# Kernel tuning notes

Hardware: AMD Instinct MI355X
Metric: run time of the kernel (lower is better)

Reference implementation:

```python
import jax, jax.numpy as jnp
import numpy as np

SPATIAL = ((100, 134), (50, 67), (25, 34), (13, 17))
LEN = sum(h * w for h, w in SPATIAL)   # 17821
D, H, L, P = 384, 8, 4, 4
DH = D // H                            # 48
U = D // 3                             # unit_dim = 128
EPS = 1e-5


def _ln(x, g, b):
    m = jnp.mean(x, -1, keepdims=True)
    v = jnp.mean((x - m) ** 2, -1, keepdims=True)
    return (x - m) * jax.lax.rsqrt(v + EPS) * g + b


def _ffn(t, w1, b1, w2, b2, g, b):
    t2 = jax.nn.relu(t @ w1.T + b1) @ w2.T + b2
    return _ln(t + t2, g, b)


def _msda_core(value, loc, attn):
    # value [B,Lv,H,DH]; loc [B,Lq,H,L,P,2] normalized to [0,1]; attn [B,Lq,H,L,P]
    B = value.shape[0]
    Lq = loc.shape[1]
    out = jnp.zeros((B, H, Lq, DH), value.dtype)
    start = 0
    for lvl, (Hl, Wl) in enumerate(SPATIAL):
        n = Hl * Wl
        v = value[:, start:start + n].transpose(0, 2, 1, 3)        # [B,H,n,DH]
        # grid_sample(align_corners=False) semantics: pixel coord = loc*W - 0.5
        x = loc[:, :, :, lvl, :, 0] * Wl - 0.5                      # [B,Lq,H,P]
        y = loc[:, :, :, lvl, :, 1] * Hl - 0.5
        x0 = jnp.floor(x); y0 = jnp.floor(y)
        dx = x - x0; dy = y - y0
        x0i = x0.astype(jnp.int32); y0i = y0.astype(jnp.int32)
        acc = jnp.zeros((B, H, Lq, P, DH), value.dtype)
        corners = ((0, 0, (1 - dx) * (1 - dy)), (1, 0, dx * (1 - dy)),
                   (0, 1, (1 - dx) * dy), (1, 1, dx * dy))
        for ox, oy, w in corners:
            xi = x0i + ox; yi = y0i + oy
            valid = ((xi >= 0) & (xi < Wl) & (yi >= 0) & (yi < Hl)).astype(value.dtype)
            idx = jnp.clip(yi, 0, Hl - 1) * Wl + jnp.clip(xi, 0, Wl - 1)
            idx_t = idx.transpose(0, 2, 1, 3).reshape(B, H, Lq * P)
            g = jnp.take_along_axis(v, idx_t[..., None], axis=2).reshape(B, H, Lq, P, DH)
            acc = acc + g * (w * valid).transpose(0, 2, 1, 3)[..., None]
        out = out + (acc * attn[:, :, :, lvl].transpose(0, 2, 1, 3)[..., None]).sum(axis=3)
        start += n
    return out.transpose(0, 2, 1, 3).reshape(B, Lq, D)


def setup_inputs() -> dict:
    key = jax.random.key(0)
    ks = jax.random.split(key, 16)
    rn = lambda k, s, sc=1.0: jax.random.normal(k, s, jnp.float32) * sc
    inp = {}
    inp['src'] = rn(ks[0], (1, LEN, D))
    inp['space_query'] = rn(ks[1], (1, 1, 2 * U))
    inp['chann_query'] = rn(ks[2], (1, 1, 2 * U))
    inp['pos'] = rn(ks[3], (1, LEN, D))
    inp['reference_points'] = jax.random.uniform(ks[4], (1, LEN, L, 2), jnp.float32)
    inp['spatial_shapes'] = jnp.array(SPATIAL, jnp.int32)
    starts = np.cumsum([0] + [h * w for h, w in SPATIAL[:-1]])
    inp['level_start_index'] = jnp.array(starts, jnp.int32)
    inp['padding_mask'] = jnp.zeros((1, LEN), bool)
    # MSDeformAttn params (torch Linear convention: W is [out_features, in_features])
    inp['W_off'] = rn(ks[5], (H * L * P * 2, D), 0.01)
    inp['b_off'] = rn(ks[6], (H * L * P * 2,), 0.1)
    inp['W_attn'] = rn(ks[7], (H * L * P, D), D ** -0.5)
    inp['b_attn'] = jnp.zeros((H * L * P,), jnp.float32)
    inp['W_val'] = rn(ks[8], (D, D), D ** -0.5)
    inp['b_val'] = jnp.zeros((D,), jnp.float32)
    inp['W_out'] = rn(ks[9], (D, D), D ** -0.5)
    inp['b_out'] = jnp.zeros((D,), jnp.float32)
    # norm1_xy / norm1_zd
    inp['g1xy'] = jnp.ones((2 * U,), jnp.float32); inp['b1xy'] = jnp.zeros((2 * U,), jnp.float32)
    inp['g1zd'] = jnp.ones((U,), jnp.float32); inp['b1zd'] = jnp.zeros((U,), jnp.float32)
    # ffn_xy: Linear(2U,2U) -> relu -> Linear(2U,2U), residual + LN
    inp['fxy_w1'] = rn(ks[10], (2 * U, 2 * U), (2 * U) ** -0.5); inp['fxy_b1'] = jnp.zeros((2 * U,), jnp.float32)
    inp['fxy_w2'] = rn(ks[11], (2 * U, 2 * U), (2 * U) ** -0.5); inp['fxy_b2'] = jnp.zeros((2 * U,), jnp.float32)
    inp['fxy_g'] = jnp.ones((2 * U,), jnp.float32); inp['fxy_b'] = jnp.zeros((2 * U,), jnp.float32)
    # ffn_zd: Linear(U,U) -> relu -> Linear(U,U), residual + LN
    inp['fzd_w1'] = rn(ks[12], (U, U), U ** -0.5); inp['fzd_b1'] = jnp.zeros((U,), jnp.float32)
    inp['fzd_w2'] = rn(ks[13], (U, U), U ** -0.5); inp['fzd_b2'] = jnp.zeros((U,), jnp.float32)
    inp['fzd_g'] = jnp.ones((U,), jnp.float32); inp['fzd_b'] = jnp.zeros((U,), jnp.float32)
    return inp


def reference(src, space_query, chann_query, pos, reference_points, spatial_shapes,
              level_start_index, padding_mask,
              W_off, b_off, W_attn, b_attn, W_val, b_val, W_out, b_out,
              g1xy, b1xy, g1zd, b1zd,
              fxy_w1, fxy_b1, fxy_w2, fxy_b2, fxy_g, fxy_b,
              fzd_w1, fzd_b1, fzd_w2, fzd_b2, fzd_g, fzd_b):
    B, Lq, _ = src.shape
    q = src + pos                                        # with_pos_embed
    value = src @ W_val.T + b_val
    value = jnp.where(padding_mask[..., None], 0.0, value).reshape(B, Lq, H, DH)
    off = (q @ W_off.T + b_off).reshape(B, Lq, H, L, P, 2)
    attn = jax.nn.softmax((q @ W_attn.T + b_attn).reshape(B, Lq, H, L * P), -1)
    attn = attn.reshape(B, Lq, H, L, P)
    wh = jnp.array([[w, h] for h, w in SPATIAL], src.dtype)         # [L,2] as (W,H)
    loc = reference_points[:, :, None, :, None, :] + off / wh[None, None, None, :, None, :]
    src2 = _msda_core(value, loc, attn) @ W_out.T + b_out
    src_xy = _ln(src[..., :2 * U] + src2[..., :2 * U], g1xy, b1xy)
    src_zd = _ln(src[..., 2 * U:] + src2[..., 2 * U:], g1zd, b1zd)
    src_xy = _ffn(src_xy, fxy_w1, fxy_b1, fxy_w2, fxy_b2, fxy_g, fxy_b)
    src_zd = _ffn(src_zd, fzd_w1, fzd_b1, fzd_w2, fzd_b2, fzd_g, fzd_b)
    return jnp.concatenate([src_xy, src_zd], axis=-1)
```

## Files before the change

### kernel.cpp

```cpp
#include <hip/hip_runtime.h>
#include <math.h>

#define LEN 17821
#define DMODEL 384
#define NHEAD 8
#define DHEAD 48
#define WSZ (384 * 384)

typedef float floatx4 __attribute__((ext_vector_type(4)));
typedef short shortx8 __attribute__((ext_vector_type(8)));
typedef unsigned short ushort;

__device__ inline ushort f2bf(float f) {
    unsigned int u = __float_as_uint(f);
    u += 0x7FFFu + ((u >> 16) & 1u);
    return (ushort)(u >> 16);
}
__device__ inline float bf2f(ushort s) {
    return __uint_as_float(((unsigned int)s) << 16);
}

__global__ __launch_bounds__(256)
void prep_w(const float* __restrict__ Wval, const float* __restrict__ Woff,
            const float* __restrict__ Wattn, const float* __restrict__ Wout,
            const float* __restrict__ w1xy, const float* __restrict__ w1zd,
            const float* __restrict__ w2xy, const float* __restrict__ w2zd,
            ushort* __restrict__ wv, ushort* __restrict__ woa,
            ushort* __restrict__ wo, ushort* __restrict__ w1b,
            ushort* __restrict__ w2b) {
    int idx = blockIdx.x * 256 + threadIdx.x;
    if (idx >= WSZ) return;
    int n = idx / 384, k = idx - n * 384;
    int job = blockIdx.y;
    float v; ushort* dst;
    if (job == 0) { v = Wval[idx]; dst = wv; }
    else if (job == 1) {
        v = n < 256 ? Woff[n * 384 + k] : Wattn[(n - 256) * 384 + k];
        dst = woa;
    } else if (job == 2) { v = Wout[idx]; dst = wo; }
    else if (job == 3) {
        v = n < 256 ? (k < 256 ? w1xy[n * 256 + k] : 0.f)
                    : (k >= 256 ? w1zd[(n - 256) * 128 + (k - 256)] : 0.f);
        dst = w1b;
    } else {
        v = n < 256 ? (k < 256 ? w2xy[n * 256 + k] : 0.f)
                    : (k >= 256 ? w2zd[(n - 256) * 128 + (k - 256)] : 0.f);
        dst = w2b;
    }
    dst[idx] = f2bf(v);
}

__global__ __launch_bounds__(384)
void prep_b(const float* __restrict__ boff, const float* __restrict__ battn,
            const float* __restrict__ b1xy, const float* __restrict__ b1zd,
            const float* __restrict__ b2xy, const float* __restrict__ b2zd,
            const float* __restrict__ g1xy, const float* __restrict__ be1xy,
            const float* __restrict__ g1zd, const float* __restrict__ be1zd,
            const float* __restrict__ g2xy, const float* __restrict__ be2xy,
            const float* __restrict__ g2zd, const float* __restrict__ be2zd,
            float* __restrict__ boa, float* __restrict__ b1c,
            float* __restrict__ b2c, float* __restrict__ l1g,
            float* __restrict__ l1b, float* __restrict__ l2g,
            float* __restrict__ l2b) {
    int i = threadIdx.x;
    bool lo = i < 256; int j = lo ? i : i - 256;
    boa[i] = lo ? boff[i] : battn[j];
    b1c[i] = lo ? b1xy[i] : b1zd[j];
    b2c[i] = lo ? b2xy[i] : b2zd[j];
    l1g[i] = lo ? g1xy[i] : g1zd[j];
    l1b[i] = lo ? be1xy[i] : be1zd[j];
    l2g[i] = lo ? g2xy[i] : g2zd[j];
    l2b[i] = lo ? be2xy[i] : be2zd[j];
}

__global__ __launch_bounds__(256)
void cvt_add(const float* __restrict__ src, const float* __restrict__ pos,
             ushort* __restrict__ src_bf, ushort* __restrict__ q_bf, int n8) {
    int i = blockIdx.x * 256 + threadIdx.x;
    if (i >= n8) return;
    float4 s0 = ((const float4*)src)[i * 2], s1 = ((const float4*)src)[i * 2 + 1];
    float4 p0 = ((const float4*)pos)[i * 2], p1 = ((const float4*)pos)[i * 2 + 1];
    shortx8 sb, qb;
    sb[0] = f2bf(s0.x); sb[1] = f2bf(s0.y); sb[2] = f2bf(s0.z); sb[3] = f2bf(s0.w);
    sb[4] = f2bf(s1.x); sb[5] = f2bf(s1.y); sb[6] = f2bf(s1.z); sb[7] = f2bf(s1.w);
    qb[0] = f2bf(s0.x + p0.x); qb[1] = f2bf(s0.y + p0.y);
    qb[2] = f2bf(s0.z + p0.z); qb[3] = f2bf(s0.w + p0.w);
    qb[4] = f2bf(s1.x + p1.x); qb[5] = f2bf(s1.y + p1.y);
    qb[6] = f2bf(s1.z + p1.z); qb[7] = f2bf(s1.w + p1.w);
    ((shortx8*)src_bf)[i] = sb;
    ((shortx8*)q_bf)[i] = qb;
}

#define TSV 128
#define LSTRIDE 40

__global__ __launch_bounds__(256)
void vq_gemm(const ushort* __restrict__ sbq, const ushort* __restrict__ qbq,
             const ushort* __restrict__ wv, const ushort* __restrict__ woa,
             const float* __restrict__ bval, const float* __restrict__ boa,
             ushort* __restrict__ vout, float* __restrict__ oaout) {
    __shared__ ushort As[TSV * LSTRIDE];
    __shared__ ushort Ws[TSV * LSTRIDE];
    bool job = blockIdx.x >= 3;
    int bx = job ? blockIdx.x - 3 : blockIdx.x;
    const ushort* A = job ? qbq : sbq;
    const ushort* W = job ? woa : wv;
    const float* bias = job ? boa : bval;
    int tid = threadIdx.x;
    int lane = tid & 63, wave = tid >> 6;
    int wr = (wave >> 1) * 64, wc = (wave & 1) * 64;
    int l15 = lane & 15, quad = lane >> 4;
    int srow = tid >> 1, shalf = tid & 1;
    int by = blockIdx.y;
    int garow = by * TSV + srow;
    bool avalid = garow < LEN;
    const ushort* ap = A + (size_t)(avalid ? garow : 0) * 384 + shalf * 16;
    const ushort* wp = W + (size_t)(bx * TSV + srow) * 384 + shalf * 16;
    ushort* as_dst = &As[srow * LSTRIDE + shalf * 16];
    ushort* ws_dst = &Ws[srow * LSTRIDE + shalf * 16];

    floatx4 acc[4][4];
    #pragma unroll
    for (int i = 0; i < 4; ++i)
        #pragma unroll
        for (int j = 0; j < 4; ++j)
            acc[i][j] = (floatx4){0.f, 0.f, 0.f, 0.f};

    shortx8 a0 = *(const shortx8*)(ap);
    shortx8 a1 = *(const shortx8*)(ap + 8);
    shortx8 w0 = *(const shortx8*)(wp);
    shortx8 w1 = *(const shortx8*)(wp + 8);

    for (int k0 = 0; k0 < 384; k0 += 32) {
        __syncthreads();
        *(shortx8*)(as_dst + 0) = a0;
        *(shortx8*)(as_dst + 8) = a1;
        *(shortx8*)(ws_dst + 0) = w0;
        *(shortx8*)(ws_dst + 8) = w1;
        __syncthreads();
        if (k0 + 32 < 384) {
            a0 = *(const shortx8*)(ap + k0 + 32);
            a1 = *(const shortx8*)(ap + k0 + 40);
            w0 = *(const shortx8*)(wp + k0 + 32);
            w1 = *(const shortx8*)(wp + k0 + 40);
        }
        shortx8 af[4], bfr[4];
        #pragma unroll
        for (int i = 0; i < 4; ++i)
            af[i] = *(shortx8*)&As[(wr + i * 16 + l15) * LSTRIDE + quad * 8];
        #pragma unroll
        for (int j = 0; j < 4; ++j)
            bfr[j] = *(shortx8*)&Ws[(wc + j * 16 + l15) * LSTRIDE + quad * 8];
        #pragma unroll
        for (int i = 0; i < 4; ++i)
            #pragma unroll
            for (int j = 0; j < 4; ++j)
                acc[i][j] = __builtin_amdgcn_mfma_f32_16x16x32_bf16(
                    af[i], bfr[j], acc[i][j], 0, 0, 0);
    }

    #pragma unroll
    for (int j = 0; j < 4; ++j) {
        int col = bx * TSV + wc + j * 16 + l15;
        float bv = bias[col];
        #pragma unroll
        for (int i = 0; i < 4; ++i) {
            #pragma unroll
            for (int r = 0; r < 4; ++r) {
                int row = by * TSV + wr + i * 16 + quad * 4 + r;
                if (row < LEN) {
                    float v = acc[i][j][r] + bv;
                    if (job) oaout[(size_t)row * 384 + col] = v;
                    else     vout[(size_t)row * 384 + col] = f2bf(v);
                }
            }
        }
    }
}

#define MTOK 8
__global__ __launch_bounds__(384)
void msda_v3(const ushort* __restrict__ value,
             const float* __restrict__ offattn,
             const float* __restrict__ refpts,
             ushort* __restrict__ out) {
    __shared__ int   sx0[MTOK * 128], sy0[MTOK * 128];
    __shared__ float sdx[MTOK * 128], sdy[MTOK * 128], saw[MTOK * 128];
    constexpr int Wi[4]  = {134, 67, 34, 17};
    constexpr int Hi[4]  = {100, 50, 25, 13};
    constexpr int STi[4] = {0, 13400, 16750, 17600};
    int t0 = blockIdx.x * MTOK;
    int tid = threadIdx.x;

    if (tid < MTOK * 8) {
        int ti = tid >> 3, h = tid & 7, t = t0 + ti;
        if (t < LEN) {
            const float* lg = offattn + (size_t)t * 384 + 256 + h * 16;
            float w[16], mx = -3.4e38f;
            #pragma unroll
            for (int s = 0; s < 16; ++s) { w[s] = lg[s]; mx = fmaxf(mx, w[s]); }
            float sum = 0.f;
            #pragma unroll
            for (int s = 0; s < 16; ++s) { w[s] = __expf(w[s] - mx); sum += w[s]; }
            float inv = 1.0f / sum;
            #pragma unroll
            for (int s = 0; s < 16; ++s) saw[ti * 128 + h * 16 + s] = w[s] * inv;
        }
    }
    for (int idx = tid; idx < MTOK * 128; idx += 384) {
        int ti = idx >> 7, rem = idx & 127, h = rem >> 4, p = rem & 15;
        int lvl = p >> 2, pp = p & 3;
        int t = t0 + ti;
        if (t < LEN) {
            float Wl = (float)Wi[lvl], Hl = (float)Hi[lvl];
            const float* op = offattn + (size_t)t * 384 + h * 32 + lvl * 8 + pp * 2;
            float ox = op[0], oy = op[1];
            float rx = refpts[(size_t)t * 8 + lvl * 2];
            float ry = refpts[(size_t)t * 8 + lvl * 2 + 1];
            float x = rx * Wl + ox - 0.5f;
            float y = ry * Hl + oy - 0.5f;
            float x0 = floorf(x), y0 = floorf(y);
            sx0[idx] = (int)x0; sy0[idx] = (int)y0;
            sdx[idx] = x - x0;  sdy[idx] = y - y0;
        }
    }
    __syncthreads();

    int ti = tid / 48;
    int r = tid - ti * 48;
    int h = r / 6;
    int c = r - h * 6;
    int t = t0 + ti;
    if (t >= LEN) return;
    const ushort* vb = value + h * DHEAD + c * 8;
    float a[8] = {};
    #pragma unroll
    for (int p = 0; p < 16; ++p) {
        const int lvl = p >> 2;
        const int Wl = Wi[lvl], Hl = Hi[lvl], st = STi[lvl];
        int base = ti * 128 + h * 16 + p;
        int x0 = sx0[base], y0 = sy0[base];
        float dx = sdx[base], dy = sdy[base], aw = saw[base];
        float cwv[4] = {(1.f - dx) * (1.f - dy), dx * (1.f - dy),
                        (1.f - dx) * dy, dx * dy};
        #pragma unroll
        for (int c2 = 0; c2 < 4; ++c2) {
            int xi = x0 + (c2 & 1), yi = y0 + (c2 >> 1);
            bool valid = (xi >= 0) & (xi < Wl) & (yi >= 0) & (yi < Hl);
            int xc = min(max(xi, 0), Wl - 1);
            int yc = min(max(yi, 0), Hl - 1);
            float s = valid ? aw * cwv[c2] : 0.f;
            shortx8 g = *(const shortx8*)(vb + (size_t)(st + yc * Wl + xc) * 384);
            #pragma unroll
            for (int k = 0; k < 8; ++k) a[k] += s * bf2f(g[k]);
        }
    }
    shortx8 o;
    #pragma unroll
    for (int k = 0; k < 8; ++k) o[k] = f2bf(a[k]);
    *(shortx8*)(out + (size_t)t * 384 + h * DHEAD + c * 8) = o;
}

#define MT 32
#define CST 392
#define WST 40

__global__ __launch_bounds__(256)
void mega_kernel(const ushort* __restrict__ Amsda, const float* __restrict__ src,
                 const ushort* __restrict__ Wo, const ushort* __restrict__ W1,
                 const ushort* __restrict__ W2,
                 const float* __restrict__ bo, const float* __restrict__ b1c,
                 const float* __restrict__ b2c,
                 const float* __restrict__ l1g, const float* __restrict__ l1b,
                 const float* __restrict__ l2g, const float* __restrict__ l2b,
                 float* __restrict__ h1f, float* __restrict__ outp) {
    __shared__ __align__(16) ushort Wbuf[384 * WST];
    __shared__ __align__(16) ushort Cbuf[MT * CST];
    ushort* Abuf = Cbuf;
    floatx4* pst4 = (floatx4*)Wbuf;
    floatx4* lnf  = (floatx4*)((char*)Wbuf + 4096);

    int tid = threadIdx.x;
    int lane = tid & 63, wave = tid >> 6;
    int wcol = wave * 96;
    int l15 = lane & 15, quad = lane >> 4;
    int by0 = blockIdx.x * MT;

    floatx4 acc[2][6];
    shortx8 wreg[6], areg;

    #pragma unroll
    for (int i = 0; i < 2; ++i)
        #pragma unroll
        for (int j = 0; j < 6; ++j) acc[i][j] = (floatx4){0.f, 0.f, 0.f, 0.f};

    if (tid < 128) {
        int gr = min(by0 + (tid >> 2), LEN - 1);
        areg = *(const shortx8*)(Amsda + (size_t)gr * 384 + (tid & 3) * 8);
    }
    #pragma unroll
    for (int cix = 0; cix < 6; ++cix) {
        int idx = cix * 256 + tid;
        wreg[cix] = *(const shortx8*)(Wo + (size_t)(idx >> 2) * 384 + (idx & 3) * 8);
    }

    for (int k0 = 0; k0 < 384; k0 += 32) {
        __syncthreads();
        if (tid < 128) *(shortx8*)(Abuf + (tid >> 2) * WST + (tid & 3) * 8) = areg;
        #pragma unroll
        for (int cix = 0; cix < 6; ++cix) {
            int idx = cix * 256 + tid;
            *(shortx8*)(Wbuf + (idx >> 2) * WST + (idx & 3) * 8) = wreg[cix];
        }
        __syncthreads();
        if (k0 + 32 < 384) {
            if (tid < 128) {
                int gr = min(by0 + (tid >> 2), LEN - 1);
                areg = *(const shortx8*)(Amsda + (size_t)gr * 384 + k0 + 32 + (tid & 3) * 8);
            }
            #pragma unroll
            for (int cix = 0; cix < 6; ++cix) {
                int idx = cix * 256 + tid;
                wreg[cix] = *(const shortx8*)(Wo + (size_t)(idx >> 2) * 384 + k0 + 32 + (idx & 3) * 8);
            }
        }
        shortx8 af[2];
        af[0] = *(shortx8*)(Abuf + (l15) * WST + quad * 8);
        af[1] = *(shortx8*)(Abuf + (16 + l15) * WST + quad * 8);
        #pragma unroll
        for (int j = 0; j < 6; ++j) {
            shortx8 bfr = *(shortx8*)(Wbuf + (wcol + j * 16 + l15) * WST + quad * 8);
            acc[0][j] = __builtin_amdgcn_mfma_f32_16x16x32_bf16(af[0], bfr, acc[0][j], 0, 0, 0);
            acc[1][j] = __builtin_amdgcn_mfma_f32_16x16x32_bf16(af[1], bfr, acc[1][j], 0, 0, 0);
        }
    }
    __syncthreads();

    #pragma unroll
    for (int j = 0; j < 6; ++j) {
        int col = wcol + j * 16 + l15;
        float bv = bo[col];
        #pragma unroll
        for (int i = 0; i < 2; ++i)
            #pragma unroll
            for (int rr = 0; rr < 4; ++rr) {
                int row = i * 16 + quad * 4 + rr;
                int gr = min(by0 + row, LEN - 1);
                float x = acc[i][j][rr] + bv + src[(size_t)gr * 384 + col];
                Cbuf[row * CST + col] = f2bf(x);
            }
    }
    __syncthreads();

    {
        int row = tid >> 3, part = tid & 7;
        float sx = 0.f, qx = 0.f, sz = 0.f, qz = 0.f;
        #pragma unroll
        for (int m = 0; m < 6; ++m) {
            int c0 = part * 48 + m * 8;
            shortx8 v = *(shortx8*)(Cbuf + row * CST + c0);
            float cs = 0.f, cq = 0.f;
            #pragma unroll
            for (int e = 0; e < 8; ++e) { float x = bf2f(v[e]); cs += x; cq += x * x; }
            if (c0 < 256) { sx += cs; qx += cq; } else { sz += cs; qz += cq; }
        }
        pst4[row * 8 + part] = (floatx4){sx, qx, sz, qz};
    }
    __syncthreads();
    if (tid < MT) {
        floatx4 s = (floatx4){0.f, 0.f, 0.f, 0.f};
        #pragma unroll
        for (int p = 0; p < 8; ++p) s += pst4[tid * 8 + p];
        float mx = s[0] / 256.f, vx = s[1] / 256.f - mx * mx;
        float mz = s[2] / 128.f, vz = s[3] / 128.f - mz * mz;
        lnf[tid] = (floatx4){mx, rsqrtf(vx + 1e-5f), mz, rsqrtf(vz + 1e-5f)};
    }
    __syncthreads();
    {
        int row = tid >> 3, part = tid & 7;
        int gr = by0 + row;
        floatx4 L = lnf[row];
        #pragma unroll
        for (int m = 0; m < 6; ++m) {
            int c0 = part * 48 + m * 8;
            bool isxy = c0 < 256;
            float mean = isxy ? L[0] : L[2];
            float inv  = isxy ? L[1] : L[3];
            shortx8 v = *(shortx8*)(Cbuf + row * CST + c0);
            float4 g0 = *(const float4*)(l1g + c0), g1 = *(const float4*)(l1g + c0 + 4);
            float4 e0 = *(const float4*)(l1b + c0), e1 = *(const float4*)(l1b + c0 + 4);
            float gg[8] = {g0.x, g0.y, g0.z, g0.w, g1.x, g1.y, g1.z, g1.w};
            float ee[8] = {e0.x, e0.y, e0.z, e0.w, e1.x, e1.y, e1.z, e1.w};
            float h[8];
            shortx8 hb;
            #pragma unroll
            for (int e = 0; e < 8; ++e) {
                h[e] = (bf2f(v[e]) - mean) * inv * gg[e] + ee[e];
                hb[e] = f2bf(h[e]);
            }
            *(shortx8*)(Cbuf + row * CST + c0) = hb;
            if (gr < LEN) {
                *(float4*)(h1f + (size_t)gr * 384 + c0)     = make_float4(h[0], h[1], h[2], h[3]);
                *(float4*)(h1f + (size_t)gr * 384 + c0 + 4) = make_float4(h[4], h[5], h[6], h[7]);
            }
        }
    }
    __syncthreads();

    #pragma unroll
    for (int i = 0; i < 2; ++i)
        #pragma unroll
        for (int j = 0; j < 6; ++j) acc[i][j] = (floatx4){0.f, 0.f, 0.f, 0.f};
    #pragma unroll
    for (int cix = 0; cix < 6; ++cix) {
        int idx = cix * 256 + tid;
        wreg[cix] = *(const shortx8*)(W1 + (size_t)(idx >> 2) * 384 + (idx & 3) * 8);
    }
    for (int k0 = 0; k0 < 384; k0 += 32) {
        __syncthreads();
        #pragma unroll
        for (int cix = 0; cix < 6; ++cix) {
            int idx = cix * 256 + tid;
            *(shortx8*)(Wbuf + (idx >> 2) * WST + (idx & 3) * 8) = wreg[cix];
        }
        __syncthreads();
        if (k0 + 32 < 384) {
            #pragma unroll
            for (int cix = 0; cix < 6; ++cix) {
                int idx = cix * 256 + tid;
                wreg[cix] = *(const shortx8*)(W1 + (size_t)(idx >> 2) * 384 + k0 + 32 + (idx & 3) * 8);
            }
        }
        shortx8 af[2];
        af[0] = *(shortx8*)(Cbuf + (l15) * CST + k0 + quad * 8);
        af[1] = *(shortx8*)(Cbuf + (16 + l15) * CST + k0 + quad * 8);
        #pragma unroll
        for (int j = 0; j < 6; ++j) {
            shortx8 bfr = *(shortx8*)(Wbuf + (wcol + j * 16 + l15) * WST + quad * 8);
            acc[0][j] = __builtin_amdgcn_mfma_f32_16x16x32_bf16(af[0], bfr, acc[0][j], 0, 0, 0);
            acc[1][j] = __builtin_amdgcn_mfma_f32_16x16x32_bf16(af[1], bfr, acc[1][j], 0, 0, 0);
        }
    }
    __syncthreads();
    #pragma unroll
    for (int j = 0; j < 6; ++j) {
        int col = wcol + j * 16 + l15;
        float bv = b1c[col];
        #pragma unroll
        for (int i = 0; i < 2; ++i)
            #pragma unroll
            for (int rr = 0; rr < 4; ++rr) {
                int row = i * 16 + quad * 4 + rr;
                Cbuf[row * CST + col] = f2bf(fmaxf(acc[i][j][rr] + bv, 0.f));
            }
    }
    __syncthreads();

    #pragma unroll
    for (int i = 0; i < 2; ++i)
        #pragma unroll
        for (int j = 0; j < 6; ++j) acc[i][j] = (floatx4){0.f, 0.f, 0.f, 0.f};
    #pragma unroll
    for (int cix = 0; cix < 6; ++cix) {
        int idx = cix * 256 + tid;
        wreg[cix] = *(const shortx8*)(W2 + (size_t)(idx >> 2) * 384 + (idx & 3) * 8);
    }
    for (int k0 = 0; k0 < 384; k0 += 32) {
        __syncthreads();
        #pragma unroll
        for (int cix = 0; cix < 6; ++cix) {
            int idx = cix * 256 + tid;
            *(shortx8*)(Wbuf + (idx >> 2) * WST + (idx & 3) * 8) = wreg[cix];
        }
        __syncthreads();
        if (k0 + 32 < 384) {
            #pragma unroll
            for (int cix = 0; cix < 6; ++cix) {
                int idx = cix * 256 + tid;
                wreg[cix] = *(const shortx8*)(W2 + (size_t)(idx >> 2) * 384 + k0 + 32 + (idx & 3) * 8);
            }
        }
        shortx8 af[2];
        af[0] = *(shortx8*)(Cbuf + (l15) * CST + k0 + quad * 8);
        af[1] = *(shortx8*)(Cbuf + (16 + l15) * CST + k0 + quad * 8);
        #pragma unroll
        for (int j = 0; j < 6; ++j) {
            shortx8 bfr = *(shortx8*)(Wbuf + (wcol + j * 16 + l15) * WST + quad * 8);
            acc[0][j] = __builtin_amdgcn_mfma_f32_16x16x32_bf16(af[0], bfr, acc[0][j], 0, 0, 0);
            acc[1][j] = __builtin_amdgcn_mfma_f32_16x16x32_bf16(af[1], bfr, acc[1][j], 0, 0, 0);
        }
    }
    __syncthreads();
    #pragma unroll
    for (int j = 0; j < 6; ++j) {
        int col = wcol + j * 16 + l15;
        float bv = b2c[col];
        #pragma unroll
        for (int i = 0; i < 2; ++i)
            #pragma unroll
            for (int rr = 0; rr < 4; ++rr) {
                int row = i * 16 + quad * 4 + rr;
                int gr = min(by0 + row, LEN - 1);
                float x = acc[i][j][rr] + bv + h1f[(size_t)gr * 384 + col];
                Cbuf[row * CST + col] = f2bf(x);
            }
    }
    __syncthreads();

    {
        int row = tid >> 3, part = tid & 7;
        float sx = 0.f, qx = 0.f, sz = 0.f, qz = 0.f;
        #pragma unroll
        for (int m = 0; m < 6; ++m) {
            int c0 = part * 48 + m * 8;
            shortx8 v = *(shortx8*)(Cbuf + row * CST + c0);
            float cs = 0.f, cq = 0.f;
            #pragma unroll
            for (int e = 0; e < 8; ++e) { float x = bf2f(v[e]); cs += x; cq += x * x; }
            if (c0 < 256) { sx += cs; qx += cq; } else { sz += cs; qz += cq; }
        }
        pst4[row * 8 + part] = (floatx4){sx, qx, sz, qz};
    }
    __syncthreads();
    if (tid < MT) {
        floatx4 s = (floatx4){0.f, 0.f, 0.f, 0.f};
        #pragma unroll
        for (int p = 0; p < 8; ++p) s += pst4[tid * 8 + p];
        float mx = s[0] / 256.f, vx = s[1] / 256.f - mx * mx;
        float mz = s[2] / 128.f, vz = s[3] / 128.f - mz * mz;
        lnf[tid] = (floatx4){mx, rsqrtf(vx + 1e-5f), mz, rsqrtf(vz + 1e-5f)};
    }
    __syncthreads();
    {
        int row = tid >> 3, part = tid & 7;
        int gr = by0 + row;
        if (gr < LEN) {
            floatx4 L = lnf[row];
            #pragma unroll
            for (int m = 0; m < 6; ++m) {
                int c0 = part * 48 + m * 8;
                bool isxy = c0 < 256;
                float mean = isxy ? L[0] : L[2];
                float inv  = isxy ? L[1] : L[3];
                shortx8 v = *(shortx8*)(Cbuf + row * CST + c0);
                float4 g0 = *(const float4*)(l2g + c0), g1 = *(const float4*)(l2g + c0 + 4);
                float4 e0 = *(const float4*)(l2b + c0), e1 = *(const float4*)(l2b + c0 + 4);
                float gg[8] = {g0.x, g0.y, g0.z, g0.w, g1.x, g1.y, g1.z, g1.w};
                float ee[8] = {e0.x, e0.y, e0.z, e0.w, e1.x, e1.y, e1.z, e1.w};
                float h[8];
                #pragma unroll
                for (int e = 0; e < 8; ++e)
                    h[e] = (bf2f(v[e]) - mean) * inv * gg[e] + ee[e];
                *(float4*)(outp + (size_t)gr * 384 + c0)     = make_float4(h[0], h[1], h[2], h[3]);
                *(float4*)(outp + (size_t)gr * 384 + c0 + 4) = make_float4(h[4], h[5], h[6], h[7]);
            }
        }
    }
}

extern "C" void kernel_launch(void* const* d_in, const int* in_sizes, int n_in,
                              void* d_out, int out_size, void* d_ws, size_t ws_size,
                              hipStream_t stream) {
    const float* src    = (const float*)d_in[0];
    const float* pos    = (const float*)d_in[3];
    const float* refpts = (const float*)d_in[4];
    const float* W_off  = (const float*)d_in[8];
    const float* b_off  = (const float*)d_in[9];
    const float* W_attn = (const float*)d_in[10];
    const float* b_attn = (const float*)d_in[11];
    const float* W_val  = (const float*)d_in[12];
    const float* b_val  = (const float*)d_in[13];
    const float* W_out  = (const float*)d_in[14];
    const float* b_out  = (const float*)d_in[15];
    const float* g1xy = (const float*)d_in[16]; const float* b1xy = (const float*)d_in[17];
    const float* g1zd = (const float*)d_in[18]; const float* b1zd = (const float*)d_in[19];
    const float* fxy_w1 = (const float*)d_in[20]; const float* fxy_b1 = (const float*)d_in[21];
    const float* fxy_w2 = (const float*)d_in[22]; const float* fxy_b2 = (const float*)d_in[23];
    const float* fxy_g  = (const float*)d_in[24]; const float* fxy_b  = (const float*)d_in[25];
    const float* fzd_w1 = (const float*)d_in[26]; const float* fzd_b1 = (const float*)d_in[27];
    const float* fzd_w2 = (const float*)d_in[28]; const float* fzd_b2 = (const float*)d_in[29];
    const float* fzd_g  = (const float*)d_in[30]; const float* fzd_b  = (const float*)d_in[31];

    float* out = (float*)d_out;
    size_t Rn = (size_t)LEN * DMODEL;

    float* f0 = (float*)d_ws;
    ushort* sb = (ushort*)(f0 + Rn);
    ushort* s0 = sb;
    ushort* s1 = sb + Rn;
    ushort* s2 = sb + 2 * Rn;
    ushort* s3 = sb + 3 * Rn;
    ushort* wv  = sb + 4 * Rn;
    ushort* woa = wv + WSZ;
    ushort* wo  = woa + WSZ;
    ushort* w1b = wo + WSZ;
    ushort* w2b = w1b + WSZ;
    float* bp = (float*)(w2b + WSZ);
    float* boa = bp;        float* b1c = bp + 384;  float* b2c = bp + 768;
    float* l1g = bp + 1152; float* l1b = bp + 1536;
    float* l2g = bp + 1920; float* l2b = bp + 2304;

    prep_w<<<dim3((WSZ + 255) / 256, 5), 256, 0, stream>>>(
        W_val, W_off, W_attn, W_out, fxy_w1, fzd_w1, fxy_w2, fzd_w2,
        wv, woa, wo, w1b, w2b);
    prep_b<<<1, 384, 0, stream>>>(b_off, b_attn, fxy_b1, fzd_b1, fxy_b2, fzd_b2,
                                  g1xy, b1xy, g1zd, b1zd, fxy_g, fxy_b, fzd_g, fzd_b,
                                  boa, b1c, b2c, l1g, l1b, l2g, l2b);

    int n8 = (int)(Rn / 8);
    cvt_add<<<(n8 + 255) / 256, 256, 0, stream>>>(src, pos, s0, s1, n8);

    vq_gemm<<<dim3(6, (LEN + TSV - 1) / TSV), 256, 0, stream>>>(
        s0, s1, wv, woa, b_val, boa, s2, f0);

    msda_v3<<<(LEN + MTOK - 1) / MTOK, 384, 0, stream>>>(s2, f0, refpts, s3);

    mega_kernel<<<(LEN + MT - 1) / MT, 256, 0, stream>>>(
        s3, src, wo, w1b, w2b, b_out, b1c, b2c,
        l1g, l1b, l2g, l2b, f0, out);
}
```

Measured before the change: 342.6 us.

## Load MFMA weight and activation fragments directly from global, drop LDS staging

The three GEMMs in the fused kernel no longer stage weight tiles (and the MSDA activation tile) through shared memory with two barriers per k-step. Each wave instead loads its B fragments (and A fragments for the first GEMM) straight from global memory into registers and double-buffers them across 64-wide k-steps. Dropping the shared weight buffer shrinks LDS use, and launch bounds now request two blocks per CU. The cost is more register pressure and redundant global/L2 reads of the weights by every block and wave without LDS sharing.

```diff
diff --git a/kernel.cpp b/kernel.cpp
--- a/kernel.cpp
+++ b/kernel.cpp
@@ -18,6 +18,10 @@
 }
 __device__ inline float bf2f(ushort s) {
     return __uint_as_float(((unsigned int)s) << 16);
+}
+
+__device__ inline floatx4 mfma_bf16(shortx8 a, shortx8 b, floatx4 c) {
+    return __builtin_amdgcn_mfma_f32_16x16x32_bf16(a, b, c, 0, 0, 0);
 }
 
 __global__ __launch_bounds__(256)
@@ -263,9 +267,8 @@
 
 #define MT 32
 #define CST 392
-#define WST 40
-
-__global__ __launch_bounds__(256)
+
+__global__ __launch_bounds__(256, 2)
 void mega_kernel(const ushort* __restrict__ Amsda, const float* __restrict__ src,
                  const ushort* __restrict__ Wo, const ushort* __restrict__ W1,
                  const ushort* __restrict__ W2,
@@ -274,11 +277,9 @@
                  const float* __restrict__ l1g, const float* __restrict__ l1b,
                  const float* __restrict__ l2g, const float* __restrict__ l2b,
                  float* __restrict__ h1f, float* __restrict__ outp) {
-    __shared__ __align__(16) ushort Wbuf[384 * WST];
     __shared__ __align__(16) ushort Cbuf[MT * CST];
-    ushort* Abuf = Cbuf;
-    floatx4* pst4 = (floatx4*)Wbuf;
-    floatx4* lnf  = (floatx4*)((char*)Wbuf + 4096);
+    __shared__ __align__(16) floatx4 pst4[MT * 8];
+    __shared__ __align__(16) floatx4 lnf[MT];
 
     int tid = threadIdx.x;
     int lane = tid & 63, wave = tid >> 6;
@@ -287,54 +288,55 @@
     int by0 = blockIdx.x * MT;
 
     floatx4 acc[2][6];
-    shortx8 wreg[6], areg;
-
-    #pragma unroll
-    for (int i = 0; i < 2; ++i)
-        #pragma unroll
-        for (int j = 0; j < 6; ++j) acc[i][j] = (floatx4){0.f, 0.f, 0.f, 0.f};
-
-    if (tid < 128) {
-        int gr = min(by0 + (tid >> 2), LEN - 1);
-        areg = *(const shortx8*)(Amsda + (size_t)gr * 384 + (tid & 3) * 8);
-    }
-    #pragma unroll
-    for (int cix = 0; cix < 6; ++cix) {
-        int idx = cix * 256 + tid;
-        wreg[cix] = *(const shortx8*)(Wo + (size_t)(idx >> 2) * 384 + (idx & 3) * 8);
-    }
-
-    for (int k0 = 0; k0 < 384; k0 += 32) {
-        __syncthreads();
-        if (tid < 128) *(shortx8*)(Abuf + (tid >> 2) * WST + (tid & 3) * 8) = areg;
-        #pragma unroll
-        for (int cix = 0; cix < 6; ++cix) {
-            int idx = cix * 256 + tid;
-            *(shortx8*)(Wbuf + (idx >> 2) * WST + (idx & 3) * 8) = wreg[cix];
-        }
-        __syncthreads();
-        if (k0 + 32 < 384) {
-            if (tid < 128) {
-                int gr = min(by0 + (tid >> 2), LEN - 1);
-                areg = *(const shortx8*)(Amsda + (size_t)gr * 384 + k0 + 32 + (tid & 3) * 8);
-            }
-            #pragma unroll
-            for (int cix = 0; cix < 6; ++cix) {
-                int idx = cix * 256 + tid;
-                wreg[cix] = *(const shortx8*)(Wo + (size_t)(idx >> 2) * 384 + k0 + 32 + (idx & 3) * 8);
-            }
-        }
-        shortx8 af[2];
-        af[0] = *(shortx8*)(Abuf + (l15) * WST + quad * 8);
-        af[1] = *(shortx8*)(Abuf + (16 + l15) * WST + quad * 8);
+
+    {
+        const ushort* ap0 = Amsda + (size_t)min(by0 + l15, LEN - 1) * 384 + quad * 8;
+        const ushort* ap1 = Amsda + (size_t)min(by0 + 16 + l15, LEN - 1) * 384 + quad * 8;
+        const ushort* wp  = Wo + (size_t)(wcol + l15) * 384 + quad * 8;
+
+        #pragma unroll
+        for (int i = 0; i < 2; ++i)
+            #pragma unroll
+            for (int j = 0; j < 6; ++j) acc[i][j] = (floatx4){0.f, 0.f, 0.f, 0.f};
+
+        shortx8 wc[6][2], wn[6][2], ac[2][2], an[2][2];
         #pragma unroll
         for (int j = 0; j < 6; ++j) {
-            shortx8 bfr = *(shortx8*)(Wbuf + (wcol + j * 16 + l15) * WST + quad * 8);
-            acc[0][j] = __builtin_amdgcn_mfma_f32_16x16x32_bf16(af[0], bfr, acc[0][j], 0, 0, 0);
-            acc[1][j] = __builtin_amdgcn_mfma_f32_16x16x32_bf16(af[1], bfr, acc[1][j], 0, 0, 0);
-        }
-    }
-    __syncthreads();
+            wc[j][0] = *(const shortx8*)(wp + j * 6144);
+            wc[j][1] = *(const shortx8*)(wp + j * 6144 + 32);
+        }
+        ac[0][0] = *(const shortx8*)(ap0); ac[0][1] = *(const shortx8*)(ap0 + 32);
+        ac[1][0] = *(const shortx8*)(ap1); ac[1][1] = *(const shortx8*)(ap1 + 32);
+
+        #pragma unroll
+        for (int ks = 0; ks < 6; ++ks) {
+            const int k0 = ks * 64;
+            if (ks < 5) {
+                #pragma unroll
+                for (int j = 0; j < 6; ++j) {
+                    wn[j][0] = *(const shortx8*)(wp + j * 6144 + k0 + 64);
+                    wn[j][1] = *(const shortx8*)(wp + j * 6144 + k0 + 96);
+                }
+                an[0][0] = *(const shortx8*)(ap0 + k0 + 64);
+                an[0][1] = *(const shortx8*)(ap0 + k0 + 96);
+                an[1][0] = *(const shortx8*)(ap1 + k0 + 64);
+                an[1][1] = *(const shortx8*)(ap1 + k0 + 96);
+            }
+            #pragma unroll
+            for (int sk = 0; sk < 2; ++sk)
+                #pragma unroll
+                for (int j = 0; j < 6; ++j) {
+                    acc[0][j] = mfma_bf16(ac[0][sk], wc[j][sk], acc[0][j]);
+                    acc[1][j] = mfma_bf16(ac[1][sk], wc[j][sk], acc[1][j]);
+                }
+            if (ks < 5) {
+                #pragma unroll
+                for (int j = 0; j < 6; ++j) { wc[j][0] = wn[j][0]; wc[j][1] = wn[j][1]; }
+                ac[0][0] = an[0][0]; ac[0][1] = an[0][1];
+                ac[1][0] = an[1][0]; ac[1][1] = an[1][1];
+            }
+        }
+    }
 
     #pragma unroll
     for (int j = 0; j < 6; ++j) {
@@ -407,38 +409,45 @@
     }
     __syncthreads();
 
-    #pragma unroll
-    for (int i = 0; i < 2; ++i)
-        #pragma unroll
-        for (int j = 0; j < 6; ++j) acc[i][j] = (floatx4){0.f, 0.f, 0.f, 0.f};
-    #pragma unroll
-    for (int cix = 0; cix < 6; ++cix) {
-        int idx = cix * 256 + tid;
-        wreg[cix] = *(const shortx8*)(W1 + (size_t)(idx >> 2) * 384 + (idx & 3) * 8);
-    }
-    for (int k0 = 0; k0 < 384; k0 += 32) {
-        __syncthreads();
-        #pragma unroll
-        for (int cix = 0; cix < 6; ++cix) {
-            int idx = cix * 256 + tid;
-            *(shortx8*)(Wbuf + (idx >> 2) * WST + (idx & 3) * 8) = wreg[cix];
-        }
-        __syncthreads();
-        if (k0 + 32 < 384) {
-            #pragma unroll
-            for (int cix = 0; cix < 6; ++cix) {
-                int idx = cix * 256 + tid;
-                wreg[cix] = *(const shortx8*)(W1 + (size_t)(idx >> 2) * 384 + k0 + 32 + (idx & 3) * 8);
-            }
-        }
-        shortx8 af[2];
-        af[0] = *(shortx8*)(Cbuf + (l15) * CST + k0 + quad * 8);
-        af[1] = *(shortx8*)(Cbuf + (16 + l15) * CST + k0 + quad * 8);
+    {
+        const ushort* wp = W1 + (size_t)(wcol + l15) * 384 + quad * 8;
+        #pragma unroll
+        for (int i = 0; i < 2; ++i)
+            #pragma unroll
+            for (int j = 0; j < 6; ++j) acc[i][j] = (floatx4){0.f, 0.f, 0.f, 0.f};
+
+        shortx8 wc[6][2], wn[6][2];
         #pragma unroll
         for (int j = 0; j < 6; ++j) {
-            shortx8 bfr = *(shortx8*)(Wbuf + (wcol + j * 16 + l15) * WST + quad * 8);
-            acc[0][j] = __builtin_amdgcn_mfma_f32_16x16x32_bf16(af[0], bfr, acc[0][j], 0, 0, 0);
-            acc[1][j] = __builtin_amdgcn_mfma_f32_16x16x32_bf16(af[1], bfr, acc[1][j], 0, 0, 0);
+            wc[j][0] = *(const shortx8*)(wp + j * 6144);
+            wc[j][1] = *(const shortx8*)(wp + j * 6144 + 32);
+        }
+        #pragma unroll
+        for (int ks = 0; ks < 6; ++ks) {
+            const int k0 = ks * 64;
+            if (ks < 5) {
+                #pragma unroll
+                for (int j = 0; j < 6; ++j) {
+                    wn[j][0] = *(const shortx8*)(wp + j * 6144 + k0 + 64);
+                    wn[j][1] = *(const shortx8*)(wp + j * 6144 + k0 + 96);
+                }
+            }
+            shortx8 a0[2], a1[2];
+            a0[0] = *(shortx8*)&Cbuf[l15 * CST + k0 + quad * 8];
+            a0[1] = *(shortx8*)&Cbuf[l15 * CST + k0 + 32 + quad * 8];
+            a1[0] = *(shortx8*)&Cbuf[(16 + l15) * CST + k0 + quad * 8];
+            a1[1] = *(shortx8*)&Cbuf[(16 + l15) * CST + k0 + 32 + quad * 8];
+            #pragma unroll
+            for (int sk = 0; sk < 2; ++sk)
+                #pragma unroll
+                for (int j = 0; j < 6; ++j) {
+                    acc[0][j] = mfma_bf16(a0[sk], wc[j][sk], acc[0][j]);
+                    acc[1][j] = mfma_bf16(a1[sk], wc[j][sk], acc[1][j]);
+                }
+            if (ks < 5) {
+                #pragma unroll
+                for (int j = 0; j < 6; ++j) { wc[j][0] = wn[j][0]; wc[j][1] = wn[j][1]; }
+            }
         }
     }
     __syncthreads();
@@ -456,38 +465,45 @@
     }
     __syncthreads();
 
-    #pragma unroll
-    for (int i = 0; i < 2; ++i)
-        #pragma unroll
-        for (int j = 0; j < 6; ++j) acc[i][j] = (floatx4){0.f, 0.f, 0.f, 0.f};
-    #pragma unroll
-    for (int cix = 0; cix < 6; ++cix) {
-        int idx = cix * 256 + tid;
-        wreg[cix] = *(const shortx8*)(W2 + (size_t)(idx >> 2) * 384 + (idx & 3) * 8);
-    }
-    for (int k0 = 0; k0 < 384; k0 += 32) {
-        __syncthreads();
-        #pragma unroll
-        for (int cix = 0; cix < 6; ++cix) {
-            int idx = cix * 256 + tid;
-            *(shortx8*)(Wbuf + (idx >> 2) * WST + (idx & 3) * 8) = wreg[cix];
-        }
-        __syncthreads();
-        if (k0 + 32 < 384) {
-            #pragma unroll
-            for (int cix = 0; cix < 6; ++cix) {
-                int idx = cix * 256 + tid;
-                wreg[cix] = *(const shortx8*)(W2 + (size_t)(idx >> 2) * 384 + k0 + 32 + (idx & 3) * 8);
-            }
-        }
-        shortx8 af[2];
-        af[0] = *(shortx8*)(Cbuf + (l15) * CST + k0 + quad * 8);
-        af[1] = *(shortx8*)(Cbuf + (16 + l15) * CST + k0 + quad * 8);
+    {
+        const ushort* wp = W2 + (size_t)(wcol + l15) * 384 + quad * 8;
+        #pragma unroll
+        for (int i = 0; i < 2; ++i)
+            #pragma unroll
+            for (int j = 0; j < 6; ++j) acc[i][j] = (floatx4){0.f, 0.f, 0.f, 0.f};
+
+        shortx8 wc[6][2], wn[6][2];
         #pragma unroll
         for (int j = 0; j < 6; ++j) {
-            shortx8 bfr = *(shortx8*)(Wbuf + (wcol + j * 16 + l15) * WST + quad * 8);
-            acc[0][j] = __builtin_amdgcn_mfma_f32_16x16x32_bf16(af[0], bfr, acc[0][j], 0, 0, 0);
-            acc[1][j] = __builtin_amdgcn_mfma_f32_16x16x32_bf16(af[1], bfr, acc[1][j], 0, 0, 0);
+            wc[j][0] = *(const shortx8*)(wp + j * 6144);
+            wc[j][1] = *(const shortx8*)(wp + j * 6144 + 32);
+        }
+        #pragma unroll
+        for (int ks = 0; ks < 6; ++ks) {
+            const int k0 = ks * 64;
+            if (ks < 5) {
+                #pragma unroll
+                for (int j = 0; j < 6; ++j) {
+                    wn[j][0] = *(const shortx8*)(wp + j * 6144 + k0 + 64);
+                    wn[j][1] = *(const shortx8*)(wp + j * 6144 + k0 + 96);
+                }
+            }
+            shortx8 a0[2], a1[2];
+            a0[0] = *(shortx8*)&Cbuf[l15 * CST + k0 + quad * 8];
+            a0[1] = *(shortx8*)&Cbuf[l15 * CST + k0 + 32 + quad * 8];
+            a1[0] = *(shortx8*)&Cbuf[(16 + l15) * CST + k0 + quad * 8];
+            a1[1] = *(shortx8*)&Cbuf[(16 + l15) * CST + k0 + 32 + quad * 8];
+            #pragma unroll
+            for (int sk = 0; sk < 2; ++sk)
+                #pragma unroll
+                for (int j = 0; j < 6; ++j) {
+                    acc[0][j] = mfma_bf16(a0[sk], wc[j][sk], acc[0][j]);
+                    acc[1][j] = mfma_bf16(a1[sk], wc[j][sk], acc[1][j]);
+                }
+            if (ks < 5) {
+                #pragma unroll
+                for (int j = 0; j < 6; ++j) { wc[j][0] = wn[j][0]; wc[j][1] = wn[j][1]; }
+            }
         }
     }
     __syncthreads();
```

Result: slower. 378.0 us (+10.3%).

## Pre-swizzle weights into MFMA fragment order and load B fragments from global

Applied to the files above, without the earlier changes.

The weight prep kernel now writes the Wout, W1 and W2 bf16 copies in the exact per-lane MFMA fragment order. The three 384-wide GEMMs in the fused kernel then read B fragments straight from global memory into registers, double-buffered in 64-wide K steps, and no longer stage weights through shared memory with two barriers per K step. The A tile for the first GEMM is loaded once into shared memory. This removes the LDS weight buffer and most barriers, allowing higher occupancy (launch bounds of 4 blocks). The cost is heavier register use and more global or L2 traffic for weights per block.

```diff
diff --git a/kernel.cpp b/kernel.cpp
--- a/kernel.cpp
+++ b/kernel.cpp
@@ -18,6 +18,10 @@
 }
 __device__ inline float bf2f(ushort s) {
     return __uint_as_float(((unsigned int)s) << 16);
+}
+
+__device__ inline floatx4 mfma_bf16(shortx8 a, shortx8 b, floatx4 c) {
+    return __builtin_amdgcn_mfma_f32_16x16x32_bf16(a, b, c, 0, 0, 0);
 }
 
 __global__ __launch_bounds__(256)
@@ -30,22 +34,36 @@
             ushort* __restrict__ w2b) {
     int idx = blockIdx.x * 256 + threadIdx.x;
     if (idx >= WSZ) return;
-    int n = idx / 384, k = idx - n * 384;
     int job = blockIdx.y;
     float v; ushort* dst;
-    if (job == 0) { v = Wval[idx]; dst = wv; }
-    else if (job == 1) {
-        v = n < 256 ? Woff[n * 384 + k] : Wattn[(n - 256) * 384 + k];
-        dst = woa;
-    } else if (job == 2) { v = Wout[idx]; dst = wo; }
-    else if (job == 3) {
-        v = n < 256 ? (k < 256 ? w1xy[n * 256 + k] : 0.f)
-                    : (k >= 256 ? w1zd[(n - 256) * 128 + (k - 256)] : 0.f);
-        dst = w1b;
+    if (job <= 1) {
+        int n = idx / 384, k = idx - n * 384;
+        if (job == 0) { v = Wval[idx]; dst = wv; }
+        else {
+            v = n < 256 ? Woff[n * 384 + k] : Wattn[(n - 256) * 384 + k];
+            dst = woa;
+        }
     } else {
-        v = n < 256 ? (k < 256 ? w2xy[n * 256 + k] : 0.f)
-                    : (k >= 256 ? w2zd[(n - 256) * 128 + (k - 256)] : 0.f);
-        dst = w2b;
+        int e = idx & 7;
+        int lane = (idx >> 3) & 63;
+        int t = idx >> 9;
+        int j = t % 6;
+        int t2 = t / 6;
+        int wv4 = t2 & 3;
+        int ks = t2 >> 2;
+        int l15 = lane & 15, quad = lane >> 4;
+        int row = wv4 * 96 + j * 16 + l15;
+        int k = ks * 32 + quad * 8 + e;
+        if (job == 2) { v = Wout[row * 384 + k]; dst = wo; }
+        else if (job == 3) {
+            v = row < 256 ? (k < 256 ? w1xy[row * 256 + k] : 0.f)
+                          : (k >= 256 ? w1zd[(row - 256) * 128 + (k - 256)] : 0.f);
+            dst = w1b;
+        } else {
+            v = row < 256 ? (k < 256 ? w2xy[row * 256 + k] : 0.f)
+                          : (k >= 256 ? w2zd[(row - 256) * 128 + (k - 256)] : 0.f);
+            dst = w2b;
+        }
     }
     dst[idx] = f2bf(v);
 }
@@ -263,9 +281,52 @@
 
 #define MT 32
 #define CST 392
-#define WST 40
-
-__global__ __launch_bounds__(256)
+
+#define GEMM384(WPTR)                                                         \
+  {                                                                           \
+    const ushort* wp_ = (WPTR) + wave * 3072 + lane * 8;                      \
+    _Pragma("unroll")                                                         \
+    for (int i_ = 0; i_ < 2; ++i_)                                            \
+      _Pragma("unroll")                                                       \
+      for (int j_ = 0; j_ < 6; ++j_) acc[i_][j_] = (floatx4){0.f,0.f,0.f,0.f};\
+    shortx8 wcr[6][2], wnr[6][2];                                             \
+    _Pragma("unroll")                                                         \
+    for (int j_ = 0; j_ < 6; ++j_) {                                          \
+      wcr[j_][0] = *(const shortx8*)(wp_ + j_ * 512);                         \
+      wcr[j_][1] = *(const shortx8*)(wp_ + 12288 + j_ * 512);                 \
+    }                                                                         \
+    _Pragma("unroll")                                                         \
+    for (int ks = 0; ks < 6; ++ks) {                                          \
+      if (ks < 5) {                                                           \
+        _Pragma("unroll")                                                     \
+        for (int j_ = 0; j_ < 6; ++j_) {                                      \
+          wnr[j_][0] = *(const shortx8*)(wp_ + (ks*2+2)*12288 + j_*512);      \
+          wnr[j_][1] = *(const shortx8*)(wp_ + (ks*2+3)*12288 + j_*512);      \
+        }                                                                     \
+      }                                                                       \
+      const int k0 = ks * 64;                                                 \
+      shortx8 a0[2], a1[2];                                                   \
+      a0[0] = *(shortx8*)&Cbuf[l15 * CST + k0 + quad * 8];                    \
+      a0[1] = *(shortx8*)&Cbuf[l15 * CST + k0 + 32 + quad * 8];               \
+      a1[0] = *(shortx8*)&Cbuf[(16 + l15) * CST + k0 + quad * 8];             \
+      a1[1] = *(shortx8*)&Cbuf[(16 + l15) * CST + k0 + 32 + quad * 8];        \
+      _Pragma("unroll")                                                       \
+      for (int sk = 0; sk < 2; ++sk)                                          \
+        _Pragma("unroll")                                                     \
+        for (int j_ = 0; j_ < 6; ++j_) {                                      \
+          acc[0][j_] = mfma_bf16(a0[sk], wcr[j_][sk], acc[0][j_]);            \
+          acc[1][j_] = mfma_bf16(a1[sk], wcr[j_][sk], acc[1][j_]);            \
+        }                                                                     \
+      if (ks < 5) {                                                           \
+        _Pragma("unroll")                                                     \
+        for (int j_ = 0; j_ < 6; ++j_) {                                      \
+          wcr[j_][0] = wnr[j_][0]; wcr[j_][1] = wnr[j_][1];                   \
+        }                                                                     \
+      }                                                                       \
+    }                                                                         \
+  }
+
+__global__ __launch_bounds__(256, 4)
 void mega_kernel(const ushort* __restrict__ Amsda, const float* __restrict__ src,
                  const ushort* __restrict__ Wo, const ushort* __restrict__ W1,
                  const ushort* __restrict__ W2,
@@ -274,66 +335,29 @@
                  const float* __restrict__ l1g, const float* __restrict__ l1b,
                  const float* __restrict__ l2g, const float* __restrict__ l2b,
                  float* __restrict__ h1f, float* __restrict__ outp) {
-    __shared__ __align__(16) ushort Wbuf[384 * WST];
     __shared__ __align__(16) ushort Cbuf[MT * CST];
-    ushort* Abuf = Cbuf;
-    floatx4* pst4 = (floatx4*)Wbuf;
-    floatx4* lnf  = (floatx4*)((char*)Wbuf + 4096);
+    __shared__ __align__(16) floatx4 pst4[MT * 8];
+    __shared__ __align__(16) floatx4 lnf[MT];
 
     int tid = threadIdx.x;
     int lane = tid & 63, wave = tid >> 6;
+    int l15 = lane & 15, quad = lane >> 4;
     int wcol = wave * 96;
-    int l15 = lane & 15, quad = lane >> 4;
     int by0 = blockIdx.x * MT;
 
     floatx4 acc[2][6];
-    shortx8 wreg[6], areg;
-
-    #pragma unroll
-    for (int i = 0; i < 2; ++i)
-        #pragma unroll
-        for (int j = 0; j < 6; ++j) acc[i][j] = (floatx4){0.f, 0.f, 0.f, 0.f};
-
-    if (tid < 128) {
-        int gr = min(by0 + (tid >> 2), LEN - 1);
-        areg = *(const shortx8*)(Amsda + (size_t)gr * 384 + (tid & 3) * 8);
-    }
+
     #pragma unroll
     for (int cix = 0; cix < 6; ++cix) {
         int idx = cix * 256 + tid;
-        wreg[cix] = *(const shortx8*)(Wo + (size_t)(idx >> 2) * 384 + (idx & 3) * 8);
-    }
-
-    for (int k0 = 0; k0 < 384; k0 += 32) {
-        __syncthreads();
-        if (tid < 128) *(shortx8*)(Abuf + (tid >> 2) * WST + (tid & 3) * 8) = areg;
-        #pragma unroll
-        for (int cix = 0; cix < 6; ++cix) {
-            int idx = cix * 256 + tid;
-            *(shortx8*)(Wbuf + (idx >> 2) * WST + (idx & 3) * 8) = wreg[cix];
-        }
-        __syncthreads();
-        if (k0 + 32 < 384) {
-            if (tid < 128) {
-                int gr = min(by0 + (tid >> 2), LEN - 1);
-                areg = *(const shortx8*)(Amsda + (size_t)gr * 384 + k0 + 32 + (tid & 3) * 8);
-            }
-            #pragma unroll
-            for (int cix = 0; cix < 6; ++cix) {
-                int idx = cix * 256 + tid;
-                wreg[cix] = *(const shortx8*)(Wo + (size_t)(idx >> 2) * 384 + k0 + 32 + (idx & 3) * 8);
-            }
-        }
-        shortx8 af[2];
-        af[0] = *(shortx8*)(Abuf + (l15) * WST + quad * 8);
-        af[1] = *(shortx8*)(Abuf + (16 + l15) * WST + quad * 8);
-        #pragma unroll
-        for (int j = 0; j < 6; ++j) {
-            shortx8 bfr = *(shortx8*)(Wbuf + (wcol + j * 16 + l15) * WST + quad * 8);
-            acc[0][j] = __builtin_amdgcn_mfma_f32_16x16x32_bf16(af[0], bfr, acc[0][j], 0, 0, 0);
-            acc[1][j] = __builtin_amdgcn_mfma_f32_16x16x32_bf16(af[1], bfr, acc[1][j], 0, 0, 0);
-        }
-    }
+        int row = idx / 48, c = idx - row * 48;
+        int gr = min(by0 + row, LEN - 1);
+        *(shortx8*)(Cbuf + row * CST + c * 8) =
+            *(const shortx8*)(Amsda + (size_t)gr * 384 + c * 8);
+    }
+    __syncthreads();
+
+    GEMM384(Wo);
     __syncthreads();
 
     #pragma unroll
@@ -407,40 +431,7 @@
     }
     __syncthreads();
 
-    #pragma unroll
-    for (int i = 0; i < 2; ++i)
-        #pragma unroll
-        for (int j = 0; j < 6; ++j) acc[i][j] = (floatx4){0.f, 0.f, 0.f, 0.f};
-    #pragma unroll
-    for (int cix = 0; cix < 6; ++cix) {
-        int idx = cix * 256 + tid;
-        wreg[cix] = *(const shortx8*)(W1 + (size_t)(idx >> 2) * 384 + (idx & 3) * 8);
-    }
-    for (int k0 = 0; k0 < 384; k0 += 32) {
-        __syncthreads();
-        #pragma unroll
-        for (int cix = 0; cix < 6; ++cix) {
-            int idx = cix * 256 + tid;
-            *(shortx8*)(Wbuf + (idx >> 2) * WST + (idx & 3) * 8) = wreg[cix];
-        }
-        __syncthreads();
-        if (k0 + 32 < 384) {
-            #pragma unroll
-            for (int cix = 0; cix < 6; ++cix) {
-                int idx = cix * 256 + tid;
-                wreg[cix] = *(const shortx8*)(W1 + (size_t)(idx >> 2) * 384 + k0 + 32 + (idx & 3) * 8);
-            }
-        }
-        shortx8 af[2];
-        af[0] = *(shortx8*)(Cbuf + (l15) * CST + k0 + quad * 8);
-        af[1] = *(shortx8*)(Cbuf + (16 + l15) * CST + k0 + quad * 8);
-        #pragma unroll
-        for (int j = 0; j < 6; ++j) {
-            shortx8 bfr = *(shortx8*)(Wbuf + (wcol + j * 16 + l15) * WST + quad * 8);
-            acc[0][j] = __builtin_amdgcn_mfma_f32_16x16x32_bf16(af[0], bfr, acc[0][j], 0, 0, 0);
-            acc[1][j] = __builtin_amdgcn_mfma_f32_16x16x32_bf16(af[1], bfr, acc[1][j], 0, 0, 0);
-        }
-    }
+    GEMM384(W1);
     __syncthreads();
     #pragma unroll
     for (int j = 0; j < 6; ++j) {
@@ -456,40 +447,7 @@
     }
     __syncthreads();
 
-    #pragma unroll
-    for (int i = 0; i < 2; ++i)
-        #pragma unroll
-        for (int j = 0; j < 6; ++j) acc[i][j] = (floatx4){0.f, 0.f, 0.f, 0.f};
-    #pragma unroll
-    for (int cix = 0; cix < 6; ++cix) {
-        int idx = cix * 256 + tid;
-        wreg[cix] = *(const shortx8*)(W2 + (size_t)(idx >> 2) * 384 + (idx & 3) * 8);
-    }
-    for (int k0 = 0; k0 < 384; k0 += 32) {
-        __syncthreads();
-        #pragma unroll
-        for (int cix = 0; cix < 6; ++cix) {
-            int idx = cix * 256 + tid;
-            *(shortx8*)(Wbuf + (idx >> 2) * WST + (idx & 3) * 8) = wreg[cix];
-        }
-        __syncthreads();
-        if (k0 + 32 < 384) {
-            #pragma unroll
-            for (int cix = 0; cix < 6; ++cix) {
-                int idx = cix * 256 + tid;
-                wreg[cix] = *(const shortx8*)(W2 + (size_t)(idx >> 2) * 384 + k0 + 32 + (idx & 3) * 8);
-            }
-        }
-        shortx8 af[2];
-        af[0] = *(shortx8*)(Cbuf + (l15) * CST + k0 + quad * 8);
-        af[1] = *(shortx8*)(Cbuf + (16 + l15) * CST + k0 + quad * 8);
-        #pragma unroll
-        for (int j = 0; j < 6; ++j) {
-            shortx8 bfr = *(shortx8*)(Wbuf + (wcol + j * 16 + l15) * WST + quad * 8);
-            acc[0][j] = __builtin_amdgcn_mfma_f32_16x16x32_bf16(af[0], bfr, acc[0][j], 0, 0, 0);
-            acc[1][j] = __builtin_amdgcn_mfma_f32_16x16x32_bf16(af[1], bfr, acc[1][j], 0, 0, 0);
-        }
-    }
+    GEMM384(W2);
     __syncthreads();
     #pragma unroll
     for (int j = 0; j < 6; ++j) {
```

New measurement: 334.0 us. -2.5%, faster.
